# Performance work log

Hardware: AMD Instinct MI355X
Metric: run time of the kernel (lower is better)

Reference implementation:

```python
import jax, jax.numpy as jnp
import numpy as np

D_MODEL = 512
N_HEADS = 8
D_K = D_MODEL // N_HEADS
D_FF = 2048
N = 4096
EPS = 1e-5


def _layer_norm(x, g, b):
    mu = jnp.mean(x, axis=-1, keepdims=True)
    var = jnp.mean(jnp.square(x - mu), axis=-1, keepdims=True)
    return (x - mu) * jax.lax.rsqrt(var + EPS) * g + b


def setup_inputs() -> dict:
    key = jax.random.key(0)
    ks = jax.random.split(key, 16)
    s = 1.0 / np.sqrt(D_MODEL)
    sf = 1.0 / np.sqrt(D_FF)
    inp = {
        "h": jax.random.normal(ks[0], (N, D_MODEL), dtype=jnp.float32),
        "adj": jax.random.randint(ks[1], (N, N), 0, 2, dtype=jnp.int32),
        "Wq": jax.random.uniform(ks[2], (D_MODEL, D_MODEL), jnp.float32, -s, s),
        "bq": jnp.zeros((D_MODEL,), jnp.float32),
        "Wk": jax.random.uniform(ks[3], (D_MODEL, D_MODEL), jnp.float32, -s, s),
        "bk": jnp.zeros((D_MODEL,), jnp.float32),
        "Wv": jax.random.uniform(ks[4], (D_MODEL, D_MODEL), jnp.float32, -s, s),
        "bv": jnp.zeros((D_MODEL,), jnp.float32),
        "Wo": jax.random.uniform(ks[5], (D_MODEL, D_MODEL), jnp.float32, -s, s),
        "bo": jnp.zeros((D_MODEL,), jnp.float32),
        "W1": jax.random.uniform(ks[6], (D_FF, D_MODEL), jnp.float32, -s, s),
        "b1": jnp.zeros((D_FF,), jnp.float32),
        "W2": jax.random.uniform(ks[7], (D_MODEL, D_FF), jnp.float32, -sf, sf),
        "b2": jnp.zeros((D_MODEL,), jnp.float32),
        "ln1_g": jnp.ones((D_MODEL,), jnp.float32),
        "ln1_b": jnp.zeros((D_MODEL,), jnp.float32),
        "ln2_g": jnp.ones((D_MODEL,), jnp.float32),
        "ln2_b": jnp.zeros((D_MODEL,), jnp.float32),
    }
    return inp


def reference(h, adj, Wq, bq, Wk, bk, Wv, bv, Wo, bo, W1, b1, W2, b2,
              ln1_g, ln1_b, ln2_g, ln2_b):
    n = h.shape[0]
    # adjacency + self loops, used as attention mask (batch=1)
    mask = adj.astype(jnp.float32) + jnp.eye(n, dtype=jnp.float32)  # [N,N]

    # QKV projections, split into heads: [N, H, Dk]
    q = (h @ Wq.T + bq).reshape(n, N_HEADS, D_K)
    k = (h @ Wk.T + bk).reshape(n, N_HEADS, D_K)
    v = (h @ Wv.T + bv).reshape(n, N_HEADS, D_K)

    scores = jnp.einsum("nhd,mhd->hnm", q, k) / jnp.sqrt(jnp.float32(D_K))
    scores = jnp.where(mask[None, :, :] == 0, jnp.float32(-1e9), scores)
    attn = jax.nn.softmax(scores, axis=-1)  # dropout is identity in eval
    ctx = jnp.einsum("hnm,mhd->nhd", attn, v).reshape(n, D_MODEL)
    attn_out = ctx @ Wo.T + bo

    h1 = _layer_norm(h + attn_out, ln1_g, ln1_b)
    ff = jax.nn.relu(h1 @ W1.T + b1) @ W2.T + b2
    h2 = _layer_norm(h1 + ff, ln2_g, ln2_b)
    return h2
```

## Files before the change

### kernel.cpp

```cpp
#include <hip/hip_runtime.h>
#include <stdint.h>
#include <stddef.h>

typedef __bf16 bf16;
typedef __bf16 bf16x8 __attribute__((ext_vector_type(8)));
typedef float  f32x4  __attribute__((ext_vector_type(4)));

typedef __attribute__((address_space(3))) void       lds_void;
typedef __attribute__((address_space(1))) const void gbl_cvoid;

#define ASYNC_CP16(g, l) \
  __builtin_amdgcn_global_load_lds((gbl_cvoid*)(g), (lds_void*)(l), 16, 0, 0)

__device__ __forceinline__ int swz(int r) { return (r & 7) ^ ((r & 8) >> 1); }

struct CastArgs {
  const float* src[7];
  bf16*        dst[7];
  int          cum[8];
};

__global__ __launch_bounds__(256) void k_prep(
    const int* __restrict__ adj, unsigned long long* __restrict__ mb,
    CastArgs a, int total8)
{
  const int bid = blockIdx.x;
  if (bid < 65536) {
    const int gw   = (int)(((unsigned)bid * 256 + threadIdx.x) >> 6);
    const int lane = threadIdx.x & 63;
    const int av   = adj[(size_t)gw * 64 + lane];
    unsigned long long m = __ballot(av != 0);
    const int row = gw >> 6, wc = gw & 63;
    if ((row >> 6) == wc) m |= 1ull << (row & 63);
    if (lane == 0) mb[gw] = m;
  } else {
    const int g = (bid - 65536) * 256 + threadIdx.x;
    if (g >= total8) return;
    int t = 0;
    while (a.cum[t + 1] <= g) ++t;
    const int i = g - a.cum[t];
    const float4* s = (const float4*)(a.src[t]) + (size_t)i * 2;
    const float4 x0 = s[0], x1 = s[1];
    bf16x8 y;
    y[0] = (bf16)x0.x; y[1] = (bf16)x0.y; y[2] = (bf16)x0.z; y[3] = (bf16)x0.w;
    y[4] = (bf16)x1.x; y[5] = (bf16)x1.y; y[6] = (bf16)x1.z; y[7] = (bf16)x1.w;
    *(bf16x8*)(a.dst[t] + (size_t)i * 8) = y;
  }
}

template <int MT>
__device__ __forceinline__ void gemm_core_async(
    const bf16* __restrict__ A, const bf16* __restrict__ B,
    bf16* As, bf16* Bs, f32x4 (&acc)[4][(MT == 128) ? 4 : 2],
    int K, int m0, int n0, int kbeg, int kend)
{
  constexpr int FN = (MT == 128) ? 4 : 2;
  constexpr int IA = MT / 32;
  const int tid    = threadIdx.x;
  const int lane   = tid & 63;
  const int wave   = tid >> 6;
  const int lane15 = lane & 15;
  const int quad   = lane >> 4;
  const int wm     = (MT == 128) ? ((wave & 1) << 6) : 0;
  const int wn     = (MT == 128) ? ((wave >> 1) << 6) : (wave << 5);

  int srA[IA], soA[IA], srB[4], soB[4];
#pragma unroll
  for (int i = 0; i < IA; ++i) {
    int c  = ((wave * IA + i) << 6) + lane;
    srA[i] = c >> 3;
    soA[i] = ((c & 7) ^ swz(srA[i])) * 8;
  }
#pragma unroll
  for (int i = 0; i < 4; ++i) {
    int c  = ((wave * 4 + i) << 6) + lane;
    srB[i] = c >> 3;
    soB[i] = ((c & 7) ^ swz(srB[i])) * 8;
  }

  const bf16* Ab = A + (size_t)m0 * K;
  const bf16* Bb = B + (size_t)n0 * K;

  for (int k0 = kbeg; k0 < kend; k0 += 64) {
#pragma unroll
    for (int i = 0; i < IA; ++i)
      ASYNC_CP16(Ab + (size_t)srA[i] * K + k0 + soA[i], &As[(wave * IA + i) * 512]);
#pragma unroll
    for (int i = 0; i < 4; ++i)
      ASYNC_CP16(Bb + (size_t)srB[i] * K + k0 + soB[i], &Bs[(wave * 4 + i) * 512]);
    __syncthreads();

#pragma unroll
    for (int kk = 0; kk < 2; ++kk) {
      bf16x8 af[4], bfr[FN];
#pragma unroll
      for (int f = 0; f < 4; ++f) {
        const int ra = wm + f * 16 + lane15;
        af[f] = *(const bf16x8*)&As[ra * 64 + (((kk * 4 + quad) ^ swz(ra)) * 8)];
      }
#pragma unroll
      for (int f = 0; f < FN; ++f) {
        const int rb = wn + f * 16 + lane15;
        bfr[f] = *(const bf16x8*)&Bs[rb * 64 + (((kk * 4 + quad) ^ swz(rb)) * 8)];
      }
#pragma unroll
      for (int fm = 0; fm < 4; ++fm)
#pragma unroll
        for (int fn = 0; fn < FN; ++fn)
          acc[fm][fn] = __builtin_amdgcn_mfma_f32_16x16x32_bf16(
              af[fm], bfr[fn], acc[fm][fn], 0, 0, 0);
    }
    __syncthreads();
  }
}

__global__ __launch_bounds__(256, 2) void k_gemm(
    const bf16* __restrict__ A, const bf16* __restrict__ B,
    const float* __restrict__ bias, bf16* __restrict__ C,
    int N, int K, int relu)
{
  __shared__ __align__(16) bf16 As[128 * 64];
  __shared__ __align__(16) bf16 Bs[128 * 64];
  const int m0 = blockIdx.x * 128, n0 = blockIdx.y * 128;
  f32x4 acc[4][4] = {};
  gemm_core_async<128>(A, B, As, Bs, acc, K, m0, n0, 0, K);

  const int lane15 = threadIdx.x & 15;
  const int quad   = (threadIdx.x & 63) >> 4;
  const int wave   = threadIdx.x >> 6;
  const int wm = (wave & 1) << 6, wn = (wave >> 1) << 6;
#pragma unroll
  for (int fm = 0; fm < 4; ++fm)
#pragma unroll
    for (int fn = 0; fn < 4; ++fn) {
      const int col = n0 + wn + fn * 16 + lane15;
      const float bv = bias[col];
#pragma unroll
      for (int r = 0; r < 4; ++r) {
        const int row = m0 + wm + fm * 16 + quad * 4 + r;
        float v = acc[fm][fn][r] + bv;
        if (relu) v = fmaxf(v, 0.0f);
        C[(size_t)row * N + col] = (bf16)v;
      }
    }
}

__global__ __launch_bounds__(256, 4) void k_gemm_qkv(
    const bf16* __restrict__ h, const bf16* __restrict__ Wcat,
    const float* __restrict__ bq, const float* __restrict__ bk,
    const float* __restrict__ bv,
    bf16* __restrict__ q, bf16* __restrict__ k, bf16* __restrict__ vt)
{
  __shared__ __align__(16) bf16 SM[64 * 64 + 128 * 64];
  bf16* As = SM;
  bf16* Bs = SM + 64 * 64;
  const int m0 = blockIdx.x * 64, n0 = blockIdx.y * 128;
  f32x4 acc[4][2] = {};
  gemm_core_async<64>(h, Wcat, As, Bs, acc, 512, m0, n0, 0, 512);

  const int lane15 = threadIdx.x & 15;
  const int quad   = (threadIdx.x & 63) >> 4;
  const int wave   = threadIdx.x >> 6;
  const int wn     = wave << 5;
  const int proj   = n0 >> 9;
  const int ncol0  = n0 & 511;
  const float* bias = (proj == 0) ? bq : (proj == 1) ? bk : bv;

  if (proj < 2) {
    bf16* C = proj ? k : q;
#pragma unroll
    for (int fm = 0; fm < 4; ++fm)
#pragma unroll
      for (int fn = 0; fn < 2; ++fn) {
        const int col = ncol0 + wn + fn * 16 + lane15;
        const float bvv = bias[col];
#pragma unroll
        for (int r = 0; r < 4; ++r) {
          const int row = m0 + fm * 16 + quad * 4 + r;
          C[(size_t)row * 512 + col] = (bf16)(acc[fm][fn][r] + bvv);
        }
      }
  } else {
    __syncthreads();
#pragma unroll
    for (int fm = 0; fm < 4; ++fm)
#pragma unroll
      for (int fn = 0; fn < 2; ++fn) {
        const int colL = wn + fn * 16 + lane15;
        const float bvv = bias[ncol0 + colL];
#pragma unroll
        for (int r = 0; r < 4; ++r) {
          const int rowL = fm * 16 + quad * 4 + r;
          SM[colL * 72 + rowL] = (bf16)(acc[fm][fn][r] + bvv);
        }
      }
    __syncthreads();
#pragma unroll
    for (int i = 0; i < 4; ++i) {
      const int c = i * 256 + threadIdx.x;
      const int colL = c >> 3, rw = (c & 7) * 8;
      *(bf16x8*)&vt[(size_t)(ncol0 + colL) * 4096 + m0 + rw] =
          *(const bf16x8*)&SM[colL * 72 + rw];
    }
  }
}

__global__ __launch_bounds__(256, 4) void k_gemm_sk(
    const bf16* __restrict__ A, const bf16* __restrict__ B,
    float* __restrict__ Cp, int N, int K, int Ksplit)
{
  __shared__ __align__(16) bf16 As[64 * 64];
  __shared__ __align__(16) bf16 Bs[128 * 64];
  const int m0 = blockIdx.x * 64, n0 = blockIdx.y * 128;
  const int kbeg = blockIdx.z * Ksplit;
  f32x4 acc[4][2] = {};
  gemm_core_async<64>(A, B, As, Bs, acc, K, m0, n0, kbeg, kbeg + Ksplit);

  const int lane15 = threadIdx.x & 15;
  const int quad   = (threadIdx.x & 63) >> 4;
  const int wave   = threadIdx.x >> 6;
  const int wn     = wave << 5;
  float* Cz = Cp + (size_t)blockIdx.z * 4096 * N;
#pragma unroll
  for (int fm = 0; fm < 4; ++fm)
#pragma unroll
    for (int fn = 0; fn < 2; ++fn) {
      const int col = n0 + wn + fn * 16 + lane15;
#pragma unroll
      for (int r = 0; r < 4; ++r) {
        const int row = m0 + fm * 16 + quad * 4 + r;
        Cz[(size_t)row * N + col] = acc[fm][fn][r];
      }
    }
}

__global__ __launch_bounds__(256, 4) void k_attn(
    const bf16* __restrict__ Q, const bf16* __restrict__ Km,
    const bf16* __restrict__ Vt, const unsigned long long* __restrict__ mb,
    bf16* __restrict__ Opart, float* __restrict__ Lpart)
{
  __shared__ __align__(16) bf16 Ks[64 * 64];
  __shared__ __align__(16) bf16 Vs[64 * 64];
  __shared__ __align__(16) bf16 Plb[4][32 * 72];

  const int tid    = threadIdx.x;
  const int wave   = tid >> 6;
  const int lane   = tid & 63;
  const int lane15 = lane & 15;
  const int quad   = lane >> 4;
  const int sp     = blockIdx.x & 3;
  const int hd     = (blockIdx.x >> 2) & 7;
  const int qt     = blockIdx.x >> 5;
  const int qrow   = qt * 128 + wave * 32;

  bf16x8 qf[2][2];
#pragma unroll
  for (int mt = 0; mt < 2; ++mt)
#pragma unroll
    for (int c = 0; c < 2; ++c)
      qf[mt][c] = *(const bf16x8*)&Q[(size_t)(qrow + mt * 16 + lane15) * 512 +
                                     hd * 64 + c * 32 + quad * 8];

  int srK[2], soK[2];
#pragma unroll
  for (int i = 0; i < 2; ++i) {
    int c  = ((wave * 2 + i) << 6) + lane;
    srK[i] = c >> 3;
    soK[i] = ((c & 7) ^ swz(srK[i])) * 8;
  }
  const bf16* KmB[2] = {
      Km + (size_t)srK[0] * 512 + hd * 64 + soK[0],
      Km + (size_t)srK[1] * 512 + hd * 64 + soK[1]};
  const bf16* VtB[2] = {
      Vt + (size_t)(hd * 64 + srK[0]) * 4096 + soK[0],
      Vt + (size_t)(hd * 64 + srK[1]) * 4096 + soK[1]};

  bf16x8 ones;
#pragma unroll
  for (int j = 0; j < 8; ++j) ones[j] = (bf16)1.0f;

  f32x4 o[2][4] = {};
  f32x4 la[2]   = {};

  for (int kt = sp * 16; kt < sp * 16 + 16; ++kt) {
    const int kb = kt * 64;
#pragma unroll
    for (int i = 0; i < 2; ++i) {
      ASYNC_CP16(KmB[i] + (size_t)kb * 512, &Ks[(wave * 2 + i) * 512]);
      ASYNC_CP16(VtB[i] + kb,               &Vs[(wave * 2 + i) * 512]);
    }
    __syncthreads();

    unsigned long long mw[2][4];
#pragma unroll
    for (int mt = 0; mt < 2; ++mt)
#pragma unroll
      for (int r = 0; r < 4; ++r)
        mw[mt][r] = mb[(size_t)(qrow + mt * 16 + quad * 4 + r) * 64 + kt] >> lane15;

#pragma unroll
    for (int g = 0; g < 4; ++g) {
      const int row = g * 16 + lane15;
      bf16x8 k0f = *(const bf16x8*)&Ks[row * 64 + ((quad       ^ swz(row)) * 8)];
      bf16x8 k1f = *(const bf16x8*)&Ks[row * 64 + (((4 + quad) ^ swz(row)) * 8)];
#pragma unroll
      for (int mt = 0; mt < 2; ++mt) {
        f32x4 s = {};
        s = __builtin_amdgcn_mfma_f32_16x16x32_bf16(qf[mt][0], k0f, s, 0, 0, 0);
        s = __builtin_amdgcn_mfma_f32_16x16x32_bf16(qf[mt][1], k1f, s, 0, 0, 0);
#pragma unroll
        for (int r = 0; r < 4; ++r) {
          const bool ok = ((mw[mt][r] >> (g * 16)) & 1ull) != 0;
          const float p = ok ? __expf(s[r] * 0.125f) : 0.0f;
          Plb[wave][(mt * 16 + quad * 4 + r) * 72 + g * 16 + lane15] = (bf16)p;
        }
      }
    }

#pragma unroll
    for (int c2 = 0; c2 < 2; ++c2) {
      bf16x8 vf[4];
#pragma unroll
      for (int g2 = 0; g2 < 4; ++g2) {
        const int row = g2 * 16 + lane15;
        vf[g2] = *(const bf16x8*)&Vs[row * 64 + (((c2 * 4 + quad) ^ swz(row)) * 8)];
      }
#pragma unroll
      for (int mt = 0; mt < 2; ++mt) {
        bf16x8 pa = *(const bf16x8*)&Plb[wave][(mt * 16 + lane15) * 72 + c2 * 32 + quad * 8];
        la[mt] = __builtin_amdgcn_mfma_f32_16x16x32_bf16(pa, ones, la[mt], 0, 0, 0);
#pragma unroll
        for (int g2 = 0; g2 < 4; ++g2)
          o[mt][g2] = __builtin_amdgcn_mfma_f32_16x16x32_bf16(pa, vf[g2], o[mt][g2], 0, 0, 0);
      }
    }
    __syncthreads();
  }

  bf16* Oz = Opart + (size_t)sp * 4096 * 512;
#pragma unroll
  for (int mt = 0; mt < 2; ++mt) {
#pragma unroll
    for (int g2 = 0; g2 < 4; ++g2)
#pragma unroll
      for (int r = 0; r < 4; ++r) {
        const int row = qrow + mt * 16 + quad * 4 + r;
        Oz[(size_t)row * 512 + hd * 64 + g2 * 16 + lane15] = (bf16)o[mt][g2][r];
      }
    if (lane15 == 0) {
#pragma unroll
      for (int r = 0; r < 4; ++r)
        Lpart[sp * 32768 + (qrow + mt * 16 + quad * 4 + r) * 8 + hd] = la[mt][r];
    }
  }
}

__global__ __launch_bounds__(256) void k_attn_combine(
    const bf16* __restrict__ Opart, const float* __restrict__ Lpart,
    bf16* __restrict__ ctx)
{
  const int g = blockIdx.x * 256 + threadIdx.x;
  const size_t base = (size_t)g * 8;
  const int row = g >> 6;
  const int hd  = (g & 63) >> 3;
  float acc[8] = {};
  float l = 0.0f;
#pragma unroll
  for (int s = 0; s < 4; ++s) {
    bf16x8 ov = *(const bf16x8*)&Opart[(size_t)s * 4096 * 512 + base];
#pragma unroll
    for (int j = 0; j < 8; ++j) acc[j] += (float)ov[j];
    l += Lpart[s * 32768 + row * 8 + hd];
  }
  const float rl = 1.0f / l;
  bf16x8 y;
#pragma unroll
  for (int j = 0; j < 8; ++j) y[j] = (bf16)(acc[j] * rl);
  *(bf16x8*)(ctx + base) = y;
}

template <int F32OUT>
__global__ __launch_bounds__(256) void k_addln_sk(
    const bf16* __restrict__ x, const float* __restrict__ Cp,
    const float* __restrict__ bias,
    const float* __restrict__ gam, const float* __restrict__ bet,
    void* __restrict__ out)
{
  const int wave = threadIdx.x >> 6, lane = threadIdx.x & 63;
  const int row  = blockIdx.x * 4 + wave;
  const size_t base = (size_t)row * 512 + lane * 8;
  const int col = lane * 8;
  bf16x8 xv = *(const bf16x8*)(x + base);
  const float* p0 = Cp + base;
  const float* p1 = Cp + (size_t)4096 * 512 + base;
  f32x4 a0 = *(const f32x4*)p0, a1 = *(const f32x4*)(p0 + 4);
  f32x4 b0 = *(const f32x4*)p1, b1 = *(const f32x4*)(p1 + 4);
  f32x4 c0 = *(const f32x4*)(bias + col), c1 = *(const f32x4*)(bias + col + 4);
  float v[8], s = 0.0f, s2 = 0.0f;
#pragma unroll
  for (int j = 0; j < 4; ++j) {
    v[j]     = (float)xv[j]     + a0[j] + b0[j] + c0[j];
    v[4 + j] = (float)xv[4 + j] + a1[j] + b1[j] + c1[j];
  }
#pragma unroll
  for (int j = 0; j < 8; ++j) { s += v[j]; s2 += v[j] * v[j]; }
#pragma unroll
  for (int d = 1; d < 64; d <<= 1) { s += __shfl_xor(s, d, 64); s2 += __shfl_xor(s2, d, 64); }
  const float mu  = s * (1.0f / 512.0f);
  const float var = s2 * (1.0f / 512.0f) - mu * mu;
  const float rs  = rsqrtf(var + 1e-5f);
  f32x4 g0 = *(const f32x4*)(gam + col), g1 = *(const f32x4*)(gam + col + 4);
  f32x4 e0 = *(const f32x4*)(bet + col), e1 = *(const f32x4*)(bet + col + 4);
  if (F32OUT) {
    float* o = (float*)out + base;
#pragma unroll
    for (int j = 0; j < 4; ++j) {
      o[j]     = ((v[j] - mu) * rs) * g0[j] + e0[j];
      o[4 + j] = ((v[4 + j] - mu) * rs) * g1[j] + e1[j];
    }
  } else {
    bf16x8 ov;
#pragma unroll
    for (int j = 0; j < 4; ++j) {
      ov[j]     = (bf16)(((v[j] - mu) * rs) * g0[j] + e0[j]);
      ov[4 + j] = (bf16)(((v[4 + j] - mu) * rs) * g1[j] + e1[j]);
    }
    *(bf16x8*)((bf16*)out + base) = ov;
  }
}

extern "C" void kernel_launch(void* const* d_in, const int* in_sizes, int n_in,
                              void* d_out, int out_size, void* d_ws, size_t ws_size,
                              hipStream_t stream)
{
  const int*   adj = (const int*)  d_in[1];
  const float* bq  = (const float*)d_in[3];
  const float* bk  = (const float*)d_in[5];
  const float* bv  = (const float*)d_in[7];
  const float* bo  = (const float*)d_in[9];
  const float* b1  = (const float*)d_in[11];
  const float* b2  = (const float*)d_in[13];
  const float* g1  = (const float*)d_in[14];
  const float* be1 = (const float*)d_in[15];
  const float* g2  = (const float*)d_in[16];
  const float* be2 = (const float*)d_in[17];

  char* ws = (char*)d_ws;
  const size_t MB = 1024 * 1024;

  bf16* hb  = (bf16*)(ws + 0 * MB);
  bf16* Wqb = (bf16*)(ws + 4 * MB);
  bf16* Wkb = (bf16*)(ws + 4 * MB + 512 * 1024);
  bf16* Wvb = (bf16*)(ws + 5 * MB);
  bf16* Wob = (bf16*)(ws + 5 * MB + 512 * 1024);
  bf16* W1b = (bf16*)(ws + 6 * MB);
  bf16* W2b = (bf16*)(ws + 8 * MB);

  bf16* q    = (bf16*)(ws + 12 * MB);
  bf16* k    = (bf16*)(ws + 16 * MB);
  bf16* vt   = (bf16*)(ws + 24 * MB);
  unsigned long long* mbits = (unsigned long long*)(ws + 28 * MB);
  bf16* ctx  = (bf16*)(ws + 30 * MB);
  bf16*  Opart = (bf16*)(ws + 34 * MB);
  float* Lpart = (float*)(ws + 50 * MB);
  float* skP   = (float*)(ws + 34 * MB);
  bf16* h1   = (bf16*)(ws + 12 * MB);
  bf16* ff1  = (bf16*)(ws + 16 * MB);

  CastArgs ca;
  const int srcIdx[7] = {0, 2, 4, 6, 8, 10, 12};
  bf16* dsts[7] = {hb, Wqb, Wkb, Wvb, Wob, W1b, W2b};
  int cum = 0;
  for (int t = 0; t < 7; ++t) {
    ca.src[t] = (const float*)d_in[srcIdx[t]];
    ca.dst[t] = dsts[t];
    ca.cum[t] = cum;
    cum += in_sizes[srcIdx[t]] / 8;
  }
  ca.cum[7] = cum;

  const dim3 blk(256);

  k_prep<<<dim3(65536 + (cum + 255) / 256), blk, 0, stream>>>(adj, mbits, ca, cum);
  k_gemm_qkv<<<dim3(64, 12), blk, 0, stream>>>(hb, Wqb, bq, bk, bv, q, k, vt);
  k_attn<<<dim3(1024), blk, 0, stream>>>(q, k, vt, mbits, Opart, Lpart);
  k_attn_combine<<<dim3(1024), blk, 0, stream>>>(Opart, Lpart, ctx);
  k_gemm_sk<<<dim3(64, 4, 2), blk, 0, stream>>>(ctx, Wob, skP, 512, 512, 256);
  k_addln_sk<0><<<dim3(1024), blk, 0, stream>>>(hb, skP, bo, g1, be1, (void*)h1);
  k_gemm<<<dim3(32, 16), blk, 0, stream>>>(h1, W1b, b1, ff1, 2048, 512, 1);
  k_gemm_sk<<<dim3(64, 4, 2), blk, 0, stream>>>(ff1, W2b, skP, 512, 2048, 1024);
  k_addln_sk<1><<<dim3(1024), blk, 0, stream>>>(h1, skP, b2, g2, be2, d_out);
}
```

Measured before the change: 291.7 us.

## Split attention block into 8 waves with 16 query rows each

The attention kernel now launches 512 threads per block, and each of 8 waves handles 16 query rows instead of 4 waves with 32 rows. K/V tile loads are spread so each wave copies one chunk. It also swaps expf for a direct exp2 with a folded scale and raises wave priority around the MFMA sequences. More waves per block is meant to improve latency hiding and cut per-wave register pressure. The cost is that each K/V fragment read from LDS is reused across half as many rows, and block barriers now span more waves.

```diff
diff --git a/kernel.cpp b/kernel.cpp
--- a/kernel.cpp
+++ b/kernel.cpp
@@ -234,14 +234,15 @@
     }
 }
 
-__global__ __launch_bounds__(256, 4) void k_attn(
+__global__ __launch_bounds__(512, 6) void k_attn(
     const bf16* __restrict__ Q, const bf16* __restrict__ Km,
     const bf16* __restrict__ Vt, const unsigned long long* __restrict__ mb,
     bf16* __restrict__ Opart, float* __restrict__ Lpart)
 {
+  constexpr int PP = 72;
   __shared__ __align__(16) bf16 Ks[64 * 64];
   __shared__ __align__(16) bf16 Vs[64 * 64];
-  __shared__ __align__(16) bf16 Plb[4][32 * 72];
+  __shared__ __align__(16) bf16 Plb[8][16 * PP];
 
   const int tid    = threadIdx.x;
   const int wave   = tid >> 6;
@@ -251,69 +252,56 @@
   const int sp     = blockIdx.x & 3;
   const int hd     = (blockIdx.x >> 2) & 7;
   const int qt     = blockIdx.x >> 5;
-  const int qrow   = qt * 128 + wave * 32;
-
-  bf16x8 qf[2][2];
-#pragma unroll
-  for (int mt = 0; mt < 2; ++mt)
-#pragma unroll
-    for (int c = 0; c < 2; ++c)
-      qf[mt][c] = *(const bf16x8*)&Q[(size_t)(qrow + mt * 16 + lane15) * 512 +
-                                     hd * 64 + c * 32 + quad * 8];
-
-  int srK[2], soK[2];
-#pragma unroll
-  for (int i = 0; i < 2; ++i) {
-    int c  = ((wave * 2 + i) << 6) + lane;
-    srK[i] = c >> 3;
-    soK[i] = ((c & 7) ^ swz(srK[i])) * 8;
-  }
-  const bf16* KmB[2] = {
-      Km + (size_t)srK[0] * 512 + hd * 64 + soK[0],
-      Km + (size_t)srK[1] * 512 + hd * 64 + soK[1]};
-  const bf16* VtB[2] = {
-      Vt + (size_t)(hd * 64 + srK[0]) * 4096 + soK[0],
-      Vt + (size_t)(hd * 64 + srK[1]) * 4096 + soK[1]};
+  const int qrow   = qt * 128 + wave * 16;
+
+  bf16x8 qf[2];
+#pragma unroll
+  for (int c = 0; c < 2; ++c)
+    qf[c] = *(const bf16x8*)&Q[(size_t)(qrow + lane15) * 512 +
+                               hd * 64 + c * 32 + quad * 8];
+
+  const int cch = (wave << 6) + lane;
+  const int sr  = cch >> 3;
+  const int so  = ((cch & 7) ^ swz(sr)) * 8;
+  const bf16* KmB = Km + (size_t)sr * 512 + hd * 64 + so;
+  const bf16* VtB = Vt + (size_t)(hd * 64 + sr) * 4096 + so;
 
   bf16x8 ones;
 #pragma unroll
   for (int j = 0; j < 8; ++j) ones[j] = (bf16)1.0f;
 
-  f32x4 o[2][4] = {};
-  f32x4 la[2]   = {};
-
-  for (int kt = sp * 16; kt < sp * 16 + 16; ++kt) {
+  f32x4 o[4] = {};
+  f32x4 la   = {};
+
+  const int kt0 = sp * 16;
+  const unsigned long long* mbw = mb + (size_t)(qrow + quad * 4) * 64;
+
+  for (int kt = kt0; kt < kt0 + 16; ++kt) {
     const int kb = kt * 64;
-#pragma unroll
-    for (int i = 0; i < 2; ++i) {
-      ASYNC_CP16(KmB[i] + (size_t)kb * 512, &Ks[(wave * 2 + i) * 512]);
-      ASYNC_CP16(VtB[i] + kb,               &Vs[(wave * 2 + i) * 512]);
-    }
-    __syncthreads();
-
-    unsigned long long mw[2][4];
-#pragma unroll
-    for (int mt = 0; mt < 2; ++mt)
-#pragma unroll
-      for (int r = 0; r < 4; ++r)
-        mw[mt][r] = mb[(size_t)(qrow + mt * 16 + quad * 4 + r) * 64 + kt] >> lane15;
+    ASYNC_CP16(KmB + (size_t)kb * 512, &Ks[wave * 512]);
+    ASYNC_CP16(VtB + kb,               &Vs[wave * 512]);
+    __syncthreads();
+
+    unsigned long long mwc[4];
+#pragma unroll
+    for (int r = 0; r < 4; ++r)
+      mwc[r] = mbw[r * 64 + kt] >> lane15;
 
 #pragma unroll
     for (int g = 0; g < 4; ++g) {
       const int row = g * 16 + lane15;
       bf16x8 k0f = *(const bf16x8*)&Ks[row * 64 + ((quad       ^ swz(row)) * 8)];
       bf16x8 k1f = *(const bf16x8*)&Ks[row * 64 + (((4 + quad) ^ swz(row)) * 8)];
-#pragma unroll
-      for (int mt = 0; mt < 2; ++mt) {
-        f32x4 s = {};
-        s = __builtin_amdgcn_mfma_f32_16x16x32_bf16(qf[mt][0], k0f, s, 0, 0, 0);
-        s = __builtin_amdgcn_mfma_f32_16x16x32_bf16(qf[mt][1], k1f, s, 0, 0, 0);
-#pragma unroll
-        for (int r = 0; r < 4; ++r) {
-          const bool ok = ((mw[mt][r] >> (g * 16)) & 1ull) != 0;
-          const float p = ok ? __expf(s[r] * 0.125f) : 0.0f;
-          Plb[wave][(mt * 16 + quad * 4 + r) * 72 + g * 16 + lane15] = (bf16)p;
-        }
+      f32x4 s = {};
+      __builtin_amdgcn_s_setprio(1);
+      s = __builtin_amdgcn_mfma_f32_16x16x32_bf16(qf[0], k0f, s, 0, 0, 0);
+      s = __builtin_amdgcn_mfma_f32_16x16x32_bf16(qf[1], k1f, s, 0, 0, 0);
+      __builtin_amdgcn_s_setprio(0);
+#pragma unroll
+      for (int r = 0; r < 4; ++r) {
+        const bool ok = ((mwc[r] >> (g * 16)) & 1ull) != 0;
+        const float p = ok ? __builtin_amdgcn_exp2f(s[r] * 0.18033688f) : 0.0f;
+        Plb[wave][(quad * 4 + r) * PP + g * 16 + lane15] = (bf16)p;
       }
     }
 
@@ -325,33 +313,29 @@
         const int row = g2 * 16 + lane15;
         vf[g2] = *(const bf16x8*)&Vs[row * 64 + (((c2 * 4 + quad) ^ swz(row)) * 8)];
       }
-#pragma unroll
-      for (int mt = 0; mt < 2; ++mt) {
-        bf16x8 pa = *(const bf16x8*)&Plb[wave][(mt * 16 + lane15) * 72 + c2 * 32 + quad * 8];
-        la[mt] = __builtin_amdgcn_mfma_f32_16x16x32_bf16(pa, ones, la[mt], 0, 0, 0);
-#pragma unroll
-        for (int g2 = 0; g2 < 4; ++g2)
-          o[mt][g2] = __builtin_amdgcn_mfma_f32_16x16x32_bf16(pa, vf[g2], o[mt][g2], 0, 0, 0);
-      }
+      bf16x8 pa = *(const bf16x8*)&Plb[wave][lane15 * PP + c2 * 32 + quad * 8];
+      __builtin_amdgcn_s_setprio(1);
+      la = __builtin_amdgcn_mfma_f32_16x16x32_bf16(pa, ones, la, 0, 0, 0);
+#pragma unroll
+      for (int g2 = 0; g2 < 4; ++g2)
+        o[g2] = __builtin_amdgcn_mfma_f32_16x16x32_bf16(pa, vf[g2], o[g2], 0, 0, 0);
+      __builtin_amdgcn_s_setprio(0);
     }
     __syncthreads();
   }
 
   bf16* Oz = Opart + (size_t)sp * 4096 * 512;
 #pragma unroll
-  for (int mt = 0; mt < 2; ++mt) {
-#pragma unroll
-    for (int g2 = 0; g2 < 4; ++g2)
-#pragma unroll
-      for (int r = 0; r < 4; ++r) {
-        const int row = qrow + mt * 16 + quad * 4 + r;
-        Oz[(size_t)row * 512 + hd * 64 + g2 * 16 + lane15] = (bf16)o[mt][g2][r];
-      }
-    if (lane15 == 0) {
-#pragma unroll
-      for (int r = 0; r < 4; ++r)
-        Lpart[sp * 32768 + (qrow + mt * 16 + quad * 4 + r) * 8 + hd] = la[mt][r];
-    }
+  for (int g2 = 0; g2 < 4; ++g2)
+#pragma unroll
+    for (int r = 0; r < 4; ++r) {
+      const int row = qrow + quad * 4 + r;
+      Oz[(size_t)row * 512 + hd * 64 + g2 * 16 + lane15] = (bf16)o[g2][r];
+    }
+  if (lane15 == 0) {
+#pragma unroll
+    for (int r = 0; r < 4; ++r)
+      Lpart[sp * 32768 + (qrow + quad * 4 + r) * 8 + hd] = la[r];
   }
 }
 
@@ -483,7 +467,7 @@
 
   k_prep<<<dim3(65536 + (cum + 255) / 256), blk, 0, stream>>>(adj, mbits, ca, cum);
   k_gemm_qkv<<<dim3(64, 12), blk, 0, stream>>>(hb, Wqb, bq, bk, bv, q, k, vt);
-  k_attn<<<dim3(1024), blk, 0, stream>>>(q, k, vt, mbits, Opart, Lpart);
+  k_attn<<<dim3(1024), dim3(512), 0, stream>>>(q, k, vt, mbits, Opart, Lpart);
   k_attn_combine<<<dim3(1024), blk, 0, stream>>>(Opart, Lpart, ctx);
   k_gemm_sk<<<dim3(64, 4, 2), blk, 0, stream>>>(ctx, Wob, skP, 512, 512, 256);
   k_addln_sk<0><<<dim3(1024), blk, 0, stream>>>(hb, skP, bo, g1, be1, (void*)h1);
```

Result: slower. 297.8 us (+2.1%).

## Fuse attention split-combine into output projection GEMM and fold softmax scale into Q

Applied to the files above, without the earlier changes.

Removes the separate attention combine kernel: a tiny kernel computes reciprocal row sums, and the Wo split-K GEMM sums the four partial outputs and normalizes them while filling its A tile. The softmax scale and log2(e) are folded into Q at the projection so the attention loop uses exp2 directly. This saves a ctx write and read plus one launch, at the cost of synchronous A loads in the GEMM and slightly different bf16 rounding of Q. Workspace buffers are rearranged to avoid overlaps.

```diff
diff --git a/kernel.cpp b/kernel.cpp
--- a/kernel.cpp
+++ b/kernel.cpp
@@ -13,6 +13,8 @@
   __builtin_amdgcn_global_load_lds((gbl_cvoid*)(g), (lds_void*)(l), 16, 0, 0)
 
 __device__ __forceinline__ int swz(int r) { return (r & 7) ^ ((r & 8) >> 1); }
+
+#define QSCALE 0.18033688f
 
 struct CastArgs {
   const float* src[7];
@@ -168,6 +170,7 @@
 
   if (proj < 2) {
     bf16* C = proj ? k : q;
+    const float sc = proj ? 1.0f : QSCALE;
 #pragma unroll
     for (int fm = 0; fm < 4; ++fm)
 #pragma unroll
@@ -177,7 +180,7 @@
 #pragma unroll
         for (int r = 0; r < 4; ++r) {
           const int row = m0 + fm * 16 + quad * 4 + r;
-          C[(size_t)row * 512 + col] = (bf16)(acc[fm][fn][r] + bvv);
+          C[(size_t)row * 512 + col] = (bf16)((acc[fm][fn][r] + bvv) * sc);
         }
       }
   } else {
@@ -230,6 +233,105 @@
       for (int r = 0; r < 4; ++r) {
         const int row = m0 + fm * 16 + quad * 4 + r;
         Cz[(size_t)row * N + col] = acc[fm][fn][r];
+      }
+    }
+}
+
+__global__ __launch_bounds__(256) void k_rl(
+    const float* __restrict__ Lpart, float* __restrict__ Rl)
+{
+  const int i = blockIdx.x * 256 + threadIdx.x;
+  const float l = Lpart[i] + Lpart[32768 + i] + Lpart[65536 + i] + Lpart[98304 + i];
+  Rl[i] = 1.0f / l;
+}
+
+__global__ __launch_bounds__(256, 4) void k_gemm_sk_ctx(
+    const bf16* __restrict__ Op, const float* __restrict__ Rl,
+    const bf16* __restrict__ B, float* __restrict__ Cp)
+{
+  __shared__ __align__(16) bf16 As[64 * 64];
+  __shared__ __align__(16) bf16 Bs[128 * 64];
+  const int tid    = threadIdx.x;
+  const int lane   = tid & 63;
+  const int wave   = tid >> 6;
+  const int lane15 = lane & 15;
+  const int quad   = lane >> 4;
+  const int m0 = blockIdx.x * 64, n0 = blockIdx.y * 128;
+  const int kbeg = blockIdx.z * 256;
+
+  int srA[2], soA[2], srB[4], soB[4];
+#pragma unroll
+  for (int i = 0; i < 2; ++i) {
+    int c  = ((wave * 2 + i) << 6) + lane;
+    srA[i] = c >> 3;
+    soA[i] = ((c & 7) ^ swz(srA[i])) * 8;
+  }
+#pragma unroll
+  for (int i = 0; i < 4; ++i) {
+    int c  = ((wave * 4 + i) << 6) + lane;
+    srB[i] = c >> 3;
+    soB[i] = ((c & 7) ^ swz(srB[i])) * 8;
+  }
+  const bf16* Bb = B + (size_t)n0 * 512;
+
+  f32x4 acc[4][2] = {};
+
+  for (int k0 = kbeg; k0 < kbeg + 256; k0 += 64) {
+#pragma unroll
+    for (int i = 0; i < 4; ++i)
+      ASYNC_CP16(Bb + (size_t)srB[i] * 512 + k0 + soB[i], &Bs[(wave * 4 + i) * 512]);
+#pragma unroll
+    for (int i = 0; i < 2; ++i) {
+      const int row = m0 + srA[i];
+      const int col = k0 + soA[i];
+      const float rl = Rl[row * 8 + (k0 >> 6)];
+      const size_t base = (size_t)row * 512 + col;
+      bf16x8 o0 = *(const bf16x8*)&Op[base];
+      bf16x8 o1 = *(const bf16x8*)&Op[(size_t)1 * 4096 * 512 + base];
+      bf16x8 o2 = *(const bf16x8*)&Op[(size_t)2 * 4096 * 512 + base];
+      bf16x8 o3 = *(const bf16x8*)&Op[(size_t)3 * 4096 * 512 + base];
+      bf16x8 y;
+#pragma unroll
+      for (int j = 0; j < 8; ++j)
+        y[j] = (bf16)(((float)o0[j] + (float)o1[j] + (float)o2[j] + (float)o3[j]) * rl);
+      *(bf16x8*)&As[(wave * 2 + i) * 512 + lane * 8] = y;
+    }
+    __syncthreads();
+
+#pragma unroll
+    for (int kk = 0; kk < 2; ++kk) {
+      bf16x8 af[4], bfr[2];
+#pragma unroll
+      for (int f = 0; f < 4; ++f) {
+        const int ra = f * 16 + lane15;
+        af[f] = *(const bf16x8*)&As[ra * 64 + (((kk * 4 + quad) ^ swz(ra)) * 8)];
+      }
+#pragma unroll
+      for (int f = 0; f < 2; ++f) {
+        const int rb = (wave << 5) + f * 16 + lane15;
+        bfr[f] = *(const bf16x8*)&Bs[rb * 64 + (((kk * 4 + quad) ^ swz(rb)) * 8)];
+      }
+#pragma unroll
+      for (int fm = 0; fm < 4; ++fm)
+#pragma unroll
+        for (int fn = 0; fn < 2; ++fn)
+          acc[fm][fn] = __builtin_amdgcn_mfma_f32_16x16x32_bf16(
+              af[fm], bfr[fn], acc[fm][fn], 0, 0, 0);
+    }
+    __syncthreads();
+  }
+
+  float* Cz = Cp + (size_t)blockIdx.z * 4096 * 512;
+  const int wn = wave << 5;
+#pragma unroll
+  for (int fm = 0; fm < 4; ++fm)
+#pragma unroll
+    for (int fn = 0; fn < 2; ++fn) {
+      const int col = n0 + wn + fn * 16 + lane15;
+#pragma unroll
+      for (int r = 0; r < 4; ++r) {
+        const int row = m0 + fm * 16 + quad * 4 + r;
+        Cz[(size_t)row * 512 + col] = acc[fm][fn][r];
       }
     }
 }
@@ -311,7 +413,7 @@
 #pragma unroll
         for (int r = 0; r < 4; ++r) {
           const bool ok = ((mw[mt][r] >> (g * 16)) & 1ull) != 0;
-          const float p = ok ? __expf(s[r] * 0.125f) : 0.0f;
+          const float p = ok ? __builtin_amdgcn_exp2f(s[r]) : 0.0f;
           Plb[wave][(mt * 16 + quad * 4 + r) * 72 + g * 16 + lane15] = (bf16)p;
         }
       }
@@ -353,30 +455,6 @@
         Lpart[sp * 32768 + (qrow + mt * 16 + quad * 4 + r) * 8 + hd] = la[mt][r];
     }
   }
-}
-
-__global__ __launch_bounds__(256) void k_attn_combine(
-    const bf16* __restrict__ Opart, const float* __restrict__ Lpart,
-    bf16* __restrict__ ctx)
-{
-  const int g = blockIdx.x * 256 + threadIdx.x;
-  const size_t base = (size_t)g * 8;
-  const int row = g >> 6;
-  const int hd  = (g & 63) >> 3;
-  float acc[8] = {};
-  float l = 0.0f;
-#pragma unroll
-  for (int s = 0; s < 4; ++s) {
-    bf16x8 ov = *(const bf16x8*)&Opart[(size_t)s * 4096 * 512 + base];
-#pragma unroll
-    for (int j = 0; j < 8; ++j) acc[j] += (float)ov[j];
-    l += Lpart[s * 32768 + row * 8 + hd];
-  }
-  const float rl = 1.0f / l;
-  bf16x8 y;
-#pragma unroll
-  for (int j = 0; j < 8; ++j) y[j] = (bf16)(acc[j] * rl);
-  *(bf16x8*)(ctx + base) = y;
 }
 
 template <int F32OUT>
@@ -460,12 +538,12 @@
   bf16* k    = (bf16*)(ws + 16 * MB);
   bf16* vt   = (bf16*)(ws + 24 * MB);
   unsigned long long* mbits = (unsigned long long*)(ws + 28 * MB);
-  bf16* ctx  = (bf16*)(ws + 30 * MB);
   bf16*  Opart = (bf16*)(ws + 34 * MB);
   float* Lpart = (float*)(ws + 50 * MB);
-  float* skP   = (float*)(ws + 34 * MB);
-  bf16* h1   = (bf16*)(ws + 12 * MB);
-  bf16* ff1  = (bf16*)(ws + 16 * MB);
+  float* Rl    = (float*)(ws + 50 * MB + 512 * 1024);
+  float* skP   = (float*)(ws + 12 * MB);
+  bf16* h1   = (bf16*)(ws + 30 * MB);
+  bf16* ff1  = (bf16*)(ws + 34 * MB);
 
   CastArgs ca;
   const int srcIdx[7] = {0, 2, 4, 6, 8, 10, 12};
@@ -484,8 +562,8 @@
   k_prep<<<dim3(65536 + (cum + 255) / 256), blk, 0, stream>>>(adj, mbits, ca, cum);
   k_gemm_qkv<<<dim3(64, 12), blk, 0, stream>>>(hb, Wqb, bq, bk, bv, q, k, vt);
   k_attn<<<dim3(1024), blk, 0, stream>>>(q, k, vt, mbits, Opart, Lpart);
-  k_attn_combine<<<dim3(1024), blk, 0, stream>>>(Opart, Lpart, ctx);
-  k_gemm_sk<<<dim3(64, 4, 2), blk, 0, stream>>>(ctx, Wob, skP, 512, 512, 256);
+  k_rl<<<dim3(128), blk, 0, stream>>>(Lpart, Rl);
+  k_gemm_sk_ctx<<<dim3(64, 4, 2), blk, 0, stream>>>(Opart, Rl, Wob, skP);
   k_addln_sk<0><<<dim3(1024), blk, 0, stream>>>(hb, skP, bo, g1, be1, (void*)h1);
   k_gemm<<<dim3(32, 16), blk, 0, stream>>>(h1, W1b, b1, ff1, 2048, 512, 1);
   k_gemm_sk<<<dim3(64, 4, 2), blk, 0, stream>>>(ff1, W2b, skP, 512, 2048, 1024);
```

Result: faster. 285.9 us (-2.0%).
